# Kernel optimization log

Hardware: AMD Instinct MI355X
Metric: run time of the kernel (lower is better)

Reference implementation:

```python
import jax, jax.numpy as jnp
import numpy as np

B, T, D, H, FA = 512, 64, 128, 128, 64


def setup_inputs() -> dict:
    key = jax.random.key(0)
    ks = jax.random.split(key, 14)
    n = lambda k, s: jax.random.normal(k, s, dtype=jnp.float32) * 0.05
    return {
        "X": jax.random.normal(ks[0], (B, T, D), dtype=jnp.float32),
        "attri_data": jax.random.normal(ks[1], (D, FA), dtype=jnp.float32),
        "w_attr1": n(ks[2], (FA, FA // 2)), "b_attr1": n(ks[3], (FA // 2,)),
        "w_attr2": n(ks[4], (FA // 2, 1)), "b_attr2": n(ks[5], (1,)),
        "w_a1": n(ks[6], (2 * H + T, H)), "b_a1": n(ks[7], (H,)),
        "w_a2": n(ks[8], (H, 1)), "b_a2": n(ks[9], (1,)),
        "w_ih": n(ks[10], (4 * H, D)), "w_hh": n(ks[11], (4 * H, H)),
        "b_ih": n(ks[12], (4 * H,)), "b_hh": n(ks[13], (4 * H,)),
    }


def reference(X, attri_data, w_attr1, b_attr1, w_attr2, b_attr2,
              w_a1, b_a1, w_a2, b_a2, w_ih, w_hh, b_ih, b_hh):
    b, t_dim, d = X.shape
    h_dim = w_hh.shape[1]

    # Attribute attention: softmax over the data_dim axis (dim=0)
    a = attri_data @ w_attr1 + b_attr1
    a = jnp.where(a > 0, a, 0.5 * a)  # LeakyReLU(negative_slope=0.5)
    alpha_attri = jax.nn.softmax(a @ w_attr2 + b_attr2, axis=0)  # [D, 1]
    X_attri = X * alpha_attri.reshape(1, 1, d)  # [B, T, D]
    Xp = jnp.transpose(X_attri, (0, 2, 1))      # [B, D, T] per-variable series

    def step(carry, x_t):  # x_t: [B, D]
        h, c = carry  # [B, H] each; state BEFORE consuming x_t (matches torch loop)
        feat = jnp.concatenate([
            jnp.broadcast_to(h[:, None, :], (b, d, h_dim)),
            jnp.broadcast_to(c[:, None, :], (b, d, h_dim)),
            Xp,
        ], axis=2)  # [B, D, 2H+T]
        e = jnp.tanh(feat @ w_a1 + b_a1) @ w_a2 + b_a2  # [B, D, 1]
        alpha_s = jax.nn.softmax(e[..., 0], axis=1)      # softmax over D
        x_tilde_t = alpha_s * x_t                        # [B, D]
        # LSTM cell (PyTorch gate order i, f, g, o)
        gates = x_t @ w_ih.T + b_ih + h @ w_hh.T + b_hh  # [B, 4H]
        i_g, f_g, g_g, o_g = jnp.split(gates, 4, axis=1)
        c_new = jax.nn.sigmoid(f_g) * c + jax.nn.sigmoid(i_g) * jnp.tanh(g_g)
        h_new = jax.nn.sigmoid(o_g) * jnp.tanh(c_new)
        return (h_new, c_new), x_tilde_t

    h0 = jnp.zeros((b, h_dim), X.dtype)
    c0 = jnp.zeros((b, h_dim), X.dtype)
    _, X_tilde = jax.lax.scan(step, (h0, c0), jnp.transpose(X_attri, (1, 0, 2)))
    return jnp.transpose(X_tilde, (1, 0, 2))  # [B, T, D]
```

## Files before the change

### kernel.cpp

```cpp
#include <hip/hip_runtime.h>
#include <hip/hip_bf16.h>
#include <cstddef>
#include <cstdint>

#define DEVI __device__ __forceinline__

typedef float f32x4 __attribute__((ext_vector_type(4)));
typedef __bf16 bf16x8 __attribute__((ext_vector_type(8)));

DEVI float fast_rcp(float x) { return __builtin_amdgcn_rcpf(x); }
DEVI float sigmoid_fast(float x) { return fast_rcp(1.0f + __expf(-x)); }
DEVI float tanh_fast(float x) { return 1.0f - 2.0f * fast_rcp(__expf(2.0f * x) + 1.0f); }
DEVI float4 ld4(const float* p) { return *reinterpret_cast<const float4*>(p); }
DEVI void st4(float* p, float4 v) { *reinterpret_cast<float4*>(p) = v; }
DEVI float f4c(const float4& v, int i) { return i == 0 ? v.x : i == 1 ? v.y : i == 2 ? v.z : v.w; }
DEVI unsigned short bfbits(float f) { return __builtin_bit_cast(unsigned short, (__bf16)f); }
DEVI unsigned pack2(float a, float b) {
  return (unsigned)bfbits(a) | ((unsigned)bfbits(b) << 16);
}
DEVI f32x4 cvt4(uint2 u) {
  f32x4 r;
  r[0] = __builtin_bit_cast(float, (u.x & 0xffffu) << 16);
  r[1] = __builtin_bit_cast(float, u.x & 0xffff0000u);
  r[2] = __builtin_bit_cast(float, (u.y & 0xffffu) << 16);
  r[3] = __builtin_bit_cast(float, u.y & 0xffff0000u);
  return r;
}
DEVI void barrier_lgkm() {
  __builtin_amdgcn_sched_barrier(0);
  asm volatile("s_waitcnt lgkmcnt(0)" ::: "memory");
  __builtin_amdgcn_s_barrier();
  __builtin_amdgcn_sched_barrier(0);
}

__global__ __launch_bounds__(128) void k_alpha(
    const float* __restrict__ AD, const float* __restrict__ W1,
    const float* __restrict__ B1, const float* __restrict__ W2,
    const float* __restrict__ B2, float* __restrict__ alpha) {
  __shared__ float sW1[64 * 32];
  __shared__ float sW2[32];
  __shared__ float sB1[32];
  __shared__ float red[128];
  __shared__ float s_mx, s_sum;
  int tid = threadIdx.x;
  for (int i = tid; i < 64 * 32; i += 128) sW1[i] = W1[i];
  if (tid < 32) { sW2[tid] = W2[tid]; sB1[tid] = B1[tid]; }
  __syncthreads();
  float ad[64];
  #pragma unroll
  for (int f = 0; f < 64; ++f) ad[f] = AD[tid * 64 + f];
  float logit = B2[0];
  #pragma unroll
  for (int j = 0; j < 32; ++j) {
    float a = sB1[j];
    #pragma unroll
    for (int f = 0; f < 64; ++f) a = fmaf(ad[f], sW1[f * 32 + j], a);
    a = a > 0.0f ? a : 0.5f * a;
    logit = fmaf(a, sW2[j], logit);
  }
  red[tid] = logit;
  __syncthreads();
  if (tid == 0) {
    float mx = red[0];
    for (int i = 1; i < 128; ++i) mx = fmaxf(mx, red[i]);
    float sm = 0.0f;
    for (int i = 0; i < 128; ++i) sm += __expf(red[i] - mx);
    s_mx = mx; s_sum = sm;
  }
  __syncthreads();
  alpha[tid] = __expf(logit - s_mx) / s_sum;
}

__global__ __launch_bounds__(256) void k_wih(
    const float* __restrict__ w_ih, const float* __restrict__ alpha,
    const float* __restrict__ b_ih, const float* __restrict__ b_hh,
    __hip_bfloat16* __restrict__ wA, float* __restrict__ biasJ) {
  int i4 = blockIdx.x * 256 + threadIdx.x;
  int j = i4 >> 5, d0 = (i4 & 31) * 4;
  float4 w = ld4(&w_ih[(size_t)j * 128 + d0]);
  float4 a = ld4(&alpha[d0]);
  uint2 o;
  o.x = pack2(w.x * a.x, w.y * a.y);
  o.y = pack2(w.z * a.z, w.w * a.w);
  *reinterpret_cast<uint2*>(&wA[(size_t)j * 128 + d0]) = o;
  if (i4 < 128) {
    int jb = i4 * 4;
    float4 v0 = ld4(&b_ih[jb]), v1 = ld4(&b_hh[jb]);
    v0.x += v1.x; v0.y += v1.y; v0.z += v1.z; v0.w += v1.w;
    st4(&biasJ[jb], v0);
  }
}

__global__ __launch_bounds__(256) void k_tw(
    const float* __restrict__ w_a1, __hip_bfloat16* __restrict__ w1T) {
  __shared__ float tile[64][132];
  int blk = blockIdx.x;
  int tid = threadIdx.x;
  #pragma unroll
  for (int i = 0; i < 32; ++i) {
    int idx = i * 256 + tid;
    int r = idx >> 7, c = idx & 127;
    tile[r][c] = w_a1[(size_t)(blk * 64 + r) * 128 + c];
  }
  __syncthreads();
  int n = tid >> 1, mh = tid & 1;
  unsigned* dst = reinterpret_cast<unsigned*>(&w1T[(size_t)n * 256 + blk * 64 + mh * 32]);
  #pragma unroll
  for (int i = 0; i < 16; ++i) {
    float a = tile[mh * 32 + 2 * i][n];
    float b = tile[mh * 32 + 2 * i + 1][n];
    dst[i] = pack2(a, b);
  }
}

__global__ __launch_bounds__(256) void k_ep(
    const float* __restrict__ X, const float* __restrict__ w_a1,
    const float* __restrict__ b_a1, const float* __restrict__ alpha,
    float* __restrict__ EP) {
  __shared__ float Xb[64][128];
  __shared__ float Wx[64][128];
  int b = blockIdx.x;
  int tid = threadIdx.x;
  #pragma unroll
  for (int i = 0; i < 8; ++i) {
    int l4 = i * 256 + tid;
    int r = l4 >> 5, c4 = l4 & 31;
    st4(&Xb[r][c4 * 4], ld4(&X[((size_t)b * 64 + r) * 128 + c4 * 4]));
    st4(&Wx[r][c4 * 4], ld4(&w_a1[(size_t)(256 + r) * 128 + c4 * 4]));
  }
  __syncthreads();
  int dg = tid & 15, kg = tid >> 4;
  float acc[8][8] = {};
  #pragma unroll 4
  for (int tau = 0; tau < 64; ++tau) {
    float4 xa0 = ld4(&Xb[tau][dg * 4]);
    float4 xa1 = ld4(&Xb[tau][64 + dg * 4]);
    float4 wa0 = ld4(&Wx[tau][kg * 4]);
    float4 wa1 = ld4(&Wx[tau][64 + kg * 4]);
    #pragma unroll
    for (int i = 0; i < 8; ++i) {
      float xv = (i < 4) ? f4c(xa0, i) : f4c(xa1, i - 4);
      #pragma unroll
      for (int j = 0; j < 4; ++j) {
        acc[i][j]     = fmaf(xv, f4c(wa0, j), acc[i][j]);
        acc[i][j + 4] = fmaf(xv, f4c(wa1, j), acc[i][j + 4]);
      }
    }
  }
  float4 ba0 = ld4(&b_a1[kg * 4]);
  float4 ba1v = ld4(&b_a1[64 + kg * 4]);
  #pragma unroll
  for (int i = 0; i < 8; ++i) {
    int drow = (i < 4) ? dg * 4 + i : 64 + dg * 4 + (i - 4);
    float al = alpha[drow];
    float4 o0, o1;
    float* p0 = &o0.x; float* p1 = &o1.x;
    #pragma unroll
    for (int j = 0; j < 4; ++j) {
      float v0 = 2.0f * fmaf(al, acc[i][j],     f4c(ba0, j));
      float v1 = 2.0f * fmaf(al, acc[i][j + 4], f4c(ba1v, j));
      p0[j] = __expf(fminf(fmaxf(v0, -40.0f), 40.0f));
      p1[j] = __expf(fminf(fmaxf(v1, -40.0f), 40.0f));
    }
    st4(&EP[((size_t)b * 128 + drow) * 128 + kg * 4], o0);
    st4(&EP[((size_t)b * 128 + drow) * 128 + 64 + kg * 4], o1);
  }
}

__global__ __launch_bounds__(256, 2) void k_gxw(
    const float* __restrict__ X, const __hip_bfloat16* __restrict__ wA,
    const float* __restrict__ biasJ, __hip_bfloat16* __restrict__ gx) {
  int rt = blockIdx.x, jt = blockIdx.y;
  int tid = threadIdx.x;
  int wv = tid >> 6, l = tid & 63, lg = l >> 4, lr = l & 15;
  int r0 = rt * 128;
  int j0 = jt * 128 + wv * 32;

  bf16x8 a[2][4];
  #pragma unroll
  for (int ri = 0; ri < 2; ++ri)
    #pragma unroll
    for (int ks = 0; ks < 4; ++ks)
      a[ri][ks] = *reinterpret_cast<const bf16x8*>(
          &wA[(size_t)(j0 + ri * 16 + lr) * 128 + ks * 32 + lg * 8]);

  f32x4 acc[2][8];
  #pragma unroll
  for (int ri = 0; ri < 2; ++ri)
    #pragma unroll
    for (int nj = 0; nj < 8; ++nj) acc[ri][nj] = (f32x4){0.f, 0.f, 0.f, 0.f};

  #pragma unroll 2
  for (int nj = 0; nj < 8; ++nj) {
    bf16x8 bh[4];
    #pragma unroll
    for (int ks = 0; ks < 4; ++ks) {
      const float* src = &X[(size_t)(r0 + nj * 16 + lr) * 128 + ks * 32 + lg * 8];
      float4 f0 = ld4(src), f1 = ld4(src + 4);
      bf16x8 fr;
      fr[0] = (__bf16)f0.x; fr[1] = (__bf16)f0.y;
      fr[2] = (__bf16)f0.z; fr[3] = (__bf16)f0.w;
      fr[4] = (__bf16)f1.x; fr[5] = (__bf16)f1.y;
      fr[6] = (__bf16)f1.z; fr[7] = (__bf16)f1.w;
      bh[ks] = fr;
    }
    #pragma unroll
    for (int ks = 0; ks < 4; ++ks) {
      acc[0][nj] = __builtin_amdgcn_mfma_f32_16x16x32_bf16(a[0][ks], bh[ks], acc[0][nj], 0, 0, 0);
      acc[1][nj] = __builtin_amdgcn_mfma_f32_16x16x32_bf16(a[1][ks], bh[ks], acc[1][nj], 0, 0, 0);
    }
  }

  #pragma unroll
  for (int ri = 0; ri < 2; ++ri) {
    int jb = j0 + ri * 16 + lg * 4;
    float4 bi = ld4(&biasJ[jb]);
    #pragma unroll
    for (int nj = 0; nj < 8; ++nj) {
      int row = r0 + nj * 16 + lr;
      uint2 o;
      o.x = pack2(acc[ri][nj][0] + bi.x, acc[ri][nj][1] + bi.y);
      o.y = pack2(acc[ri][nj][2] + bi.z, acc[ri][nj][3] + bi.w);
      *reinterpret_cast<uint2*>(&gx[(size_t)row * 512 + jb]) = o;
    }
  }
}

__global__ __launch_bounds__(512, 1) void k_rec(
    const __hip_bfloat16* __restrict__ gx, const float* __restrict__ w_hh,
    __hip_bfloat16* __restrict__ S) {
  __shared__ unsigned short kB[2][16 * 128];
  int tid = threadIdx.x;
  int wv = tid >> 6, l = tid & 63, lg = l >> 4, lr = l & 15;
  int b0 = blockIdx.x * 16;

  bf16x8 ah[4][4];
  #pragma unroll
  for (int ks = 0; ks < 4; ++ks)
    #pragma unroll
    for (int q = 0; q < 4; ++q) {
      const float* src = &w_hh[(size_t)(q * 128 + wv * 16 + lr) * 128 + ks * 32 + lg * 8];
      float4 f0 = ld4(src), f1 = ld4(src + 4);
      bf16x8 fr;
      fr[0] = (__bf16)f0.x; fr[1] = (__bf16)f0.y;
      fr[2] = (__bf16)f0.z; fr[3] = (__bf16)f0.w;
      fr[4] = (__bf16)f1.x; fr[5] = (__bf16)f1.y;
      fr[6] = (__bf16)f1.z; fr[7] = (__bf16)f1.w;
      ah[ks][q] = fr;
    }

  alignas(16) float hA[4] = {0.f, 0.f, 0.f, 0.f};
  alignas(16) float cA[4] = {0.f, 0.f, 0.f, 0.f};
  int m0 = wv * 16 + lg * 4;
  int wIdx = lr * 128 + (((m0 >> 3) ^ lr) << 3) + (m0 & 7);
  const __hip_bfloat16* gxb = gx + (size_t)(b0 + lr) * 64 * 512 + wv * 16 + lg * 4;

  uint2 z; z.x = 0u; z.y = 0u;
  *reinterpret_cast<uint2*>(&kB[0][wIdx]) = z;
  uint2 gA[4], gB[4];
  #pragma unroll
  for (int q = 0; q < 4; ++q) gA[q] = *reinterpret_cast<const uint2*>(gxb + q * 128);
  #pragma unroll
  for (int q = 0; q < 4; ++q) gB[q] = *reinterpret_cast<const uint2*>(gxb + 512 + q * 128);
  __syncthreads();

#define REC_STEP(T, SRC, DST, G)                                               \
  do {                                                                         \
    int t_ = (T);                                                              \
    bf16x8 bh[4];                                                              \
    _Pragma("unroll")                                                          \
    for (int ks = 0; ks < 4; ++ks)                                             \
      bh[ks] = *reinterpret_cast<const bf16x8*>(                               \
          &kB[SRC][lr * 128 + ((((ks << 2) + lg) ^ lr) << 3)]);                \
    f32x4 ac0 = cvt4(G[0]), ac1 = cvt4(G[1]), ac2 = cvt4(G[2]), ac3 = cvt4(G[3]); \
    int tn_ = t_ + 2 < 64 ? t_ + 2 : 63;                                       \
    _Pragma("unroll")                                                          \
    for (int q = 0; q < 4; ++q)                                                \
      G[q] = *reinterpret_cast<const uint2*>(gxb + (size_t)tn_ * 512 + q * 128); \
    {                                                                          \
      uint2 hS; hS.x = pack2(hA[0], hA[1]); hS.y = pack2(hA[2], hA[3]);        \
      uint2 cS; cS.x = pack2(cA[0], cA[1]); cS.y = pack2(cA[2], cA[3]);        \
      __hip_bfloat16* sp = S + ((size_t)(t_ * 512) + b0 + lr) * 256 + m0;      \
      *reinterpret_cast<uint2*>(sp) = hS;                                      \
      *reinterpret_cast<uint2*>(sp + 128) = cS;                                \
    }                                                                          \
    _Pragma("unroll")                                                          \
    for (int ks = 0; ks < 4; ++ks) {                                           \
      ac0 = __builtin_amdgcn_mfma_f32_16x16x32_bf16(ah[ks][0], bh[ks], ac0, 0, 0, 0); \
      ac1 = __builtin_amdgcn_mfma_f32_16x16x32_bf16(ah[ks][1], bh[ks], ac1, 0, 0, 0); \
      ac2 = __builtin_amdgcn_mfma_f32_16x16x32_bf16(ah[ks][2], bh[ks], ac2, 0, 0, 0); \
      ac3 = __builtin_amdgcn_mfma_f32_16x16x32_bf16(ah[ks][3], bh[ks], ac3, 0, 0, 0); \
    }                                                                          \
    _Pragma("unroll")                                                          \
    for (int r = 0; r < 4; ++r) {                                              \
      float ig = sigmoid_fast(ac0[r]);                                         \
      float fg = sigmoid_fast(ac1[r]);                                         \
      float gg = tanh_fast(ac2[r]);                                            \
      float og = sigmoid_fast(ac3[r]);                                         \
      float cn = fmaf(fg, cA[r], ig * gg);                                     \
      float hn = og * tanh_fast(cn);                                           \
      cA[r] = cn; hA[r] = hn;                                                  \
    }                                                                          \
    {                                                                          \
      uint2 hu; hu.x = pack2(hA[0], hA[1]); hu.y = pack2(hA[2], hA[3]);        \
      *reinterpret_cast<uint2*>(&kB[DST][wIdx]) = hu;                          \
    }                                                                          \
    barrier_lgkm();                                                            \
  } while (0)

  #pragma unroll 1
  for (int it = 0; it < 32; ++it) {
    REC_STEP(2 * it, 0, 1, gA);
    REC_STEP(2 * it + 1, 1, 0, gB);
  }
#undef REC_STEP
}

__global__ __launch_bounds__(256, 1) void k_eq(
    const __hip_bfloat16* __restrict__ S, const __hip_bfloat16* __restrict__ w1T,
    float* __restrict__ EQ) {
  int tid = threadIdx.x;
  int wv = tid >> 6, l = tid & 63;
  int lr = l & 15, lg = l >> 4;
  int r0 = blockIdx.x * 128 + wv * 32;

  bf16x8 a[2][8];
  #pragma unroll
  for (int ri = 0; ri < 2; ++ri)
    #pragma unroll
    for (int ks = 0; ks < 8; ++ks)
      a[ri][ks] = *reinterpret_cast<const bf16x8*>(
          &S[(size_t)(r0 + ri * 16 + lr) * 256 + ks * 32 + lg * 8]);

  f32x4 acc[2][8];
  #pragma unroll
  for (int ri = 0; ri < 2; ++ri)
    #pragma unroll
    for (int nj = 0; nj < 8; ++nj) acc[ri][nj] = (f32x4){0.f, 0.f, 0.f, 0.f};

  #pragma unroll
  for (int nj = 0; nj < 8; ++nj) {
    bf16x8 bf[8];
    #pragma unroll
    for (int ks = 0; ks < 8; ++ks)
      bf[ks] = *reinterpret_cast<const bf16x8*>(
          &w1T[(size_t)(nj * 16 + lr) * 256 + ks * 32 + lg * 8]);
    #pragma unroll
    for (int ks = 0; ks < 8; ++ks) {
      acc[0][nj] = __builtin_amdgcn_mfma_f32_16x16x32_bf16(a[0][ks], bf[ks], acc[0][nj], 0, 0, 0);
      acc[1][nj] = __builtin_amdgcn_mfma_f32_16x16x32_bf16(a[1][ks], bf[ks], acc[1][nj], 0, 0, 0);
    }
  }

  #pragma unroll
  for (int ri = 0; ri < 2; ++ri)
    #pragma unroll
    for (int nj = 0; nj < 8; ++nj)
      #pragma unroll
      for (int r = 0; r < 4; ++r) {
        int grow = r0 + ri * 16 + lg * 4 + r;
        int n = nj * 16 + lr;
        float v = 2.0f * acc[ri][nj][r];
        EQ[(size_t)grow * 128 + n] = __expf(fminf(fmaxf(v, -40.f), 40.f));
      }
}

__global__ __launch_bounds__(512, 2) void k_attn(
    const float* __restrict__ EP, const float* __restrict__ EQ,
    const float* __restrict__ w_a2, const float* __restrict__ alpha,
    const float* __restrict__ X, float* __restrict__ out) {
  __shared__ float EQs[64][128];
  __shared__ float e_lds[8][128];
  int b = blockIdx.x;
  int tid = threadIdx.x;
  #pragma unroll
  for (int i = 0; i < 4; ++i) {
    int l4 = i * 512 + tid;
    int t = l4 >> 5, k4 = l4 & 31;
    st4(&EQs[t][k4 * 4], ld4(&EQ[((size_t)t * 512 + b) * 128 + k4 * 4]));
  }
  int d = tid >> 2, s = tid & 3;
  float4 ep[8], w2r[8];
  #pragma unroll
  for (int q = 0; q < 8; ++q) {
    ep[q]  = ld4(&EP[((size_t)b * 128 + d) * 128 + s * 32 + q * 4]);
    w2r[q] = ld4(&w_a2[s * 32 + q * 4]);
  }
  int wv = tid >> 6, l = tid & 63;
  float al0 = alpha[l], al1 = alpha[64 + l];
  barrier_lgkm();

  for (int rnd = 0; rnd < 8; ++rnd) {
    #pragma unroll
    for (int it = 0; it < 8; ++it) {
      int t = rnd * 8 + it;
      float p = 0.0f;
      #pragma unroll
      for (int q = 0; q < 8; ++q) {
        float4 eq = ld4(&EQs[t][s * 32 + q * 4]);
        p = fmaf(w2r[q].x, fast_rcp(fmaf(ep[q].x, eq.x, 1.0f)), p);
        p = fmaf(w2r[q].y, fast_rcp(fmaf(ep[q].y, eq.y, 1.0f)), p);
        p = fmaf(w2r[q].z, fast_rcp(fmaf(ep[q].z, eq.z, 1.0f)), p);
        p = fmaf(w2r[q].w, fast_rcp(fmaf(ep[q].w, eq.w, 1.0f)), p);
      }
      p += __shfl_xor(p, 1);
      p += __shfl_xor(p, 2);
      if (s == 0) e_lds[it][d] = -2.0f * p;
    }
    barrier_lgkm();
    {
      int t = rnd * 8 + wv;
      float v0 = e_lds[wv][l], v1 = e_lds[wv][64 + l];
      float mx = fmaxf(v0, v1);
      #pragma unroll
      for (int o = 1; o < 64; o <<= 1) mx = fmaxf(mx, __shfl_xor(mx, o));
      float e0 = __expf(v0 - mx), e1 = __expf(v1 - mx);
      float sm = e0 + e1;
      #pragma unroll
      for (int o = 1; o < 64; o <<= 1) sm += __shfl_xor(sm, o);
      float inv = fast_rcp(sm);
      size_t ro = ((size_t)b * 64 + t) * 128;
      out[ro + l]      = e0 * inv * al0 * X[ro + l];
      out[ro + 64 + l] = e1 * inv * al1 * X[ro + 64 + l];
    }
    barrier_lgkm();
  }
}

extern "C" void kernel_launch(void* const* d_in, const int* in_sizes, int n_in,
                              void* d_out, int out_size, void* d_ws, size_t ws_size,
                              hipStream_t stream) {
  const float* X    = (const float*)d_in[0];
  const float* AD   = (const float*)d_in[1];
  const float* W1   = (const float*)d_in[2];
  const float* B1   = (const float*)d_in[3];
  const float* W2   = (const float*)d_in[4];
  const float* B2   = (const float*)d_in[5];
  const float* w_a1 = (const float*)d_in[6];
  const float* b_a1 = (const float*)d_in[7];
  const float* w_a2 = (const float*)d_in[8];
  const float* w_ih = (const float*)d_in[10];
  const float* w_hh = (const float*)d_in[11];
  const float* b_ih = (const float*)d_in[12];
  const float* b_hh = (const float*)d_in[13];
  float* out = (float*)d_out;
  float* ws = (float*)d_ws;

  float* alpha = ws;
  float* EQ    = ws + 256;
  float* EP    = EQ + 4194304;
  float* fS    = EP + 8388608;
  __hip_bfloat16* S = (__hip_bfloat16*)fS;
  float* fgx   = fS + 4194304;
  __hip_bfloat16* gx = (__hip_bfloat16*)fgx;
  float* fw1T  = fgx + 8388608;
  __hip_bfloat16* w1T = (__hip_bfloat16*)fw1T;
  float* fwA   = fw1T + 16384;
  __hip_bfloat16* wA = (__hip_bfloat16*)fwA;
  float* biasJ = fwA + 32768;

  hipLaunchKernelGGL(k_alpha, dim3(1),   dim3(128), 0, stream, AD, W1, B1, W2, B2, alpha);
  hipLaunchKernelGGL(k_wih,   dim3(64),  dim3(256), 0, stream, w_ih, alpha, b_ih, b_hh, wA, biasJ);
  hipLaunchKernelGGL(k_tw,    dim3(4),   dim3(256), 0, stream, w_a1, w1T);
  hipLaunchKernelGGL(k_ep,    dim3(512), dim3(256), 0, stream, X, w_a1, b_a1, alpha, EP);
  hipLaunchKernelGGL(k_gxw,   dim3(256, 4), dim3(256), 0, stream, X, wA, biasJ, gx);
  hipLaunchKernelGGL(k_rec,   dim3(32),  dim3(512), 0, stream, gx, w_hh, S);
  hipLaunchKernelGGL(k_eq,    dim3(256), dim3(256), 0, stream, S, w1T, EQ);
  hipLaunchKernelGGL(k_attn,  dim3(512), dim3(512), 0, stream, EP, EQ, w_a2, alpha, X, out);
}
```

Before: 362.9 us.

## Fuse prep kernels, fold EQ projection into recurrence, co-schedule EP blocks

Merges the alpha, w_ih scaling and w_a1 transpose kernels into one prep launch, with each block recomputing alpha redundantly. The hidden/cell state projection that produced EQ now runs inside the recurrent kernel through extra MFMAs on the LDS-resident h and c, which removes the S buffer round trip and the separate k_eq launch. The EP computation runs as extra blocks of the same launch so it can overlap the 32 latency-bound recurrence blocks. The cost is more work and LDS traffic per recurrence step on the serial critical path, plus redundant alpha computation in 64 blocks.

```diff
diff --git a/kernel.cpp b/kernel.cpp
--- a/kernel.cpp
+++ b/kernel.cpp
@@ -33,137 +33,87 @@
   __builtin_amdgcn_sched_barrier(0);
 }
 
-__global__ __launch_bounds__(128) void k_alpha(
+__global__ __launch_bounds__(256) void k_prep(
     const float* __restrict__ AD, const float* __restrict__ W1,
     const float* __restrict__ B1, const float* __restrict__ W2,
-    const float* __restrict__ B2, float* __restrict__ alpha) {
-  __shared__ float sW1[64 * 32];
-  __shared__ float sW2[32];
-  __shared__ float sB1[32];
-  __shared__ float red[128];
-  __shared__ float s_mx, s_sum;
-  int tid = threadIdx.x;
-  for (int i = tid; i < 64 * 32; i += 128) sW1[i] = W1[i];
-  if (tid < 32) { sW2[tid] = W2[tid]; sB1[tid] = B1[tid]; }
-  __syncthreads();
-  float ad[64];
-  #pragma unroll
-  for (int f = 0; f < 64; ++f) ad[f] = AD[tid * 64 + f];
-  float logit = B2[0];
-  #pragma unroll
-  for (int j = 0; j < 32; ++j) {
-    float a = sB1[j];
-    #pragma unroll
-    for (int f = 0; f < 64; ++f) a = fmaf(ad[f], sW1[f * 32 + j], a);
-    a = a > 0.0f ? a : 0.5f * a;
-    logit = fmaf(a, sW2[j], logit);
-  }
-  red[tid] = logit;
-  __syncthreads();
-  if (tid == 0) {
-    float mx = red[0];
-    for (int i = 1; i < 128; ++i) mx = fmaxf(mx, red[i]);
-    float sm = 0.0f;
-    for (int i = 0; i < 128; ++i) sm += __expf(red[i] - mx);
-    s_mx = mx; s_sum = sm;
-  }
-  __syncthreads();
-  alpha[tid] = __expf(logit - s_mx) / s_sum;
-}
-
-__global__ __launch_bounds__(256) void k_wih(
-    const float* __restrict__ w_ih, const float* __restrict__ alpha,
+    const float* __restrict__ B2, const float* __restrict__ w_ih,
     const float* __restrict__ b_ih, const float* __restrict__ b_hh,
-    __hip_bfloat16* __restrict__ wA, float* __restrict__ biasJ) {
-  int i4 = blockIdx.x * 256 + threadIdx.x;
-  int j = i4 >> 5, d0 = (i4 & 31) * 4;
-  float4 w = ld4(&w_ih[(size_t)j * 128 + d0]);
-  float4 a = ld4(&alpha[d0]);
-  uint2 o;
-  o.x = pack2(w.x * a.x, w.y * a.y);
-  o.y = pack2(w.z * a.z, w.w * a.w);
-  *reinterpret_cast<uint2*>(&wA[(size_t)j * 128 + d0]) = o;
-  if (i4 < 128) {
-    int jb = i4 * 4;
-    float4 v0 = ld4(&b_ih[jb]), v1 = ld4(&b_hh[jb]);
-    v0.x += v1.x; v0.y += v1.y; v0.z += v1.z; v0.w += v1.w;
-    st4(&biasJ[jb], v0);
-  }
-}
-
-__global__ __launch_bounds__(256) void k_tw(
-    const float* __restrict__ w_a1, __hip_bfloat16* __restrict__ w1T) {
-  __shared__ float tile[64][132];
-  int blk = blockIdx.x;
-  int tid = threadIdx.x;
-  #pragma unroll
-  for (int i = 0; i < 32; ++i) {
-    int idx = i * 256 + tid;
-    int r = idx >> 7, c = idx & 127;
-    tile[r][c] = w_a1[(size_t)(blk * 64 + r) * 128 + c];
-  }
-  __syncthreads();
-  int n = tid >> 1, mh = tid & 1;
-  unsigned* dst = reinterpret_cast<unsigned*>(&w1T[(size_t)n * 256 + blk * 64 + mh * 32]);
-  #pragma unroll
-  for (int i = 0; i < 16; ++i) {
-    float a = tile[mh * 32 + 2 * i][n];
-    float b = tile[mh * 32 + 2 * i + 1][n];
-    dst[i] = pack2(a, b);
-  }
-}
-
-__global__ __launch_bounds__(256) void k_ep(
-    const float* __restrict__ X, const float* __restrict__ w_a1,
-    const float* __restrict__ b_a1, const float* __restrict__ alpha,
-    float* __restrict__ EP) {
-  __shared__ float Xb[64][128];
-  __shared__ float Wx[64][128];
-  int b = blockIdx.x;
-  int tid = threadIdx.x;
-  #pragma unroll
-  for (int i = 0; i < 8; ++i) {
-    int l4 = i * 256 + tid;
-    int r = l4 >> 5, c4 = l4 & 31;
-    st4(&Xb[r][c4 * 4], ld4(&X[((size_t)b * 64 + r) * 128 + c4 * 4]));
-    st4(&Wx[r][c4 * 4], ld4(&w_a1[(size_t)(256 + r) * 128 + c4 * 4]));
-  }
-  __syncthreads();
-  int dg = tid & 15, kg = tid >> 4;
-  float acc[8][8] = {};
-  #pragma unroll 4
-  for (int tau = 0; tau < 64; ++tau) {
-    float4 xa0 = ld4(&Xb[tau][dg * 4]);
-    float4 xa1 = ld4(&Xb[tau][64 + dg * 4]);
-    float4 wa0 = ld4(&Wx[tau][kg * 4]);
-    float4 wa1 = ld4(&Wx[tau][64 + kg * 4]);
-    #pragma unroll
-    for (int i = 0; i < 8; ++i) {
-      float xv = (i < 4) ? f4c(xa0, i) : f4c(xa1, i - 4);
-      #pragma unroll
-      for (int j = 0; j < 4; ++j) {
-        acc[i][j]     = fmaf(xv, f4c(wa0, j), acc[i][j]);
-        acc[i][j + 4] = fmaf(xv, f4c(wa1, j), acc[i][j + 4]);
+    const float* __restrict__ w_a1, float* __restrict__ alpha_g,
+    __hip_bfloat16* __restrict__ wA, float* __restrict__ biasJ,
+    __hip_bfloat16* __restrict__ w1T) {
+  __shared__ float sh[64 * 132];
+  int bid = blockIdx.x, tid = threadIdx.x;
+  if (bid < 64) {
+    float* sW1 = sh;
+    float* sW2 = sh + 2048;
+    float* sB1 = sh + 2080;
+    float* red = sh + 2112;
+    float* sA  = sh + 2240;
+    float* sMS = sh + 2368;
+    for (int i = tid; i < 2048; i += 256) sW1[i] = W1[i];
+    if (tid < 32) { sW2[tid] = W2[tid]; sB1[tid] = B1[tid]; }
+    __syncthreads();
+    if (tid < 128) {
+      float ad[64];
+      #pragma unroll
+      for (int f = 0; f < 64; ++f) ad[f] = AD[tid * 64 + f];
+      float logit = B2[0];
+      #pragma unroll
+      for (int j = 0; j < 32; ++j) {
+        float a = sB1[j];
+        #pragma unroll
+        for (int f = 0; f < 64; ++f) a = fmaf(ad[f], sW1[f * 32 + j], a);
+        a = a > 0.0f ? a : 0.5f * a;
+        logit = fmaf(a, sW2[j], logit);
       }
-    }
-  }
-  float4 ba0 = ld4(&b_a1[kg * 4]);
-  float4 ba1v = ld4(&b_a1[64 + kg * 4]);
-  #pragma unroll
-  for (int i = 0; i < 8; ++i) {
-    int drow = (i < 4) ? dg * 4 + i : 64 + dg * 4 + (i - 4);
-    float al = alpha[drow];
-    float4 o0, o1;
-    float* p0 = &o0.x; float* p1 = &o1.x;
-    #pragma unroll
-    for (int j = 0; j < 4; ++j) {
-      float v0 = 2.0f * fmaf(al, acc[i][j],     f4c(ba0, j));
-      float v1 = 2.0f * fmaf(al, acc[i][j + 4], f4c(ba1v, j));
-      p0[j] = __expf(fminf(fmaxf(v0, -40.0f), 40.0f));
-      p1[j] = __expf(fminf(fmaxf(v1, -40.0f), 40.0f));
-    }
-    st4(&EP[((size_t)b * 128 + drow) * 128 + kg * 4], o0);
-    st4(&EP[((size_t)b * 128 + drow) * 128 + 64 + kg * 4], o1);
+      red[tid] = logit;
+    }
+    __syncthreads();
+    if (tid == 0) {
+      float mx = red[0];
+      for (int i = 1; i < 128; ++i) mx = fmaxf(mx, red[i]);
+      float sm = 0.0f;
+      for (int i = 0; i < 128; ++i) sm += __expf(red[i] - mx);
+      sMS[0] = mx; sMS[1] = sm;
+    }
+    __syncthreads();
+    if (tid < 128) {
+      float a = __expf(red[tid] - sMS[0]) / sMS[1];
+      sA[tid] = a;
+      if (bid == 0) alpha_g[tid] = a;
+    }
+    __syncthreads();
+    int i4 = bid * 256 + tid;
+    int j = i4 >> 5, d0 = (i4 & 31) * 4;
+    float4 w = ld4(&w_ih[(size_t)j * 128 + d0]);
+    uint2 o;
+    o.x = pack2(w.x * sA[d0], w.y * sA[d0 + 1]);
+    o.y = pack2(w.z * sA[d0 + 2], w.w * sA[d0 + 3]);
+    *reinterpret_cast<uint2*>(&wA[(size_t)j * 128 + d0]) = o;
+    if (i4 < 128) {
+      int jb = i4 * 4;
+      float4 v0 = ld4(&b_ih[jb]), v1 = ld4(&b_hh[jb]);
+      v0.x += v1.x; v0.y += v1.y; v0.z += v1.z; v0.w += v1.w;
+      st4(&biasJ[jb], v0);
+    }
+  } else {
+    float (*tile)[132] = reinterpret_cast<float(*)[132]>(sh);
+    int blk = bid - 64;
+    #pragma unroll
+    for (int i = 0; i < 32; ++i) {
+      int idx = i * 256 + tid;
+      int r = idx >> 7, c = idx & 127;
+      tile[r][c] = w_a1[(size_t)(blk * 64 + r) * 128 + c];
+    }
+    __syncthreads();
+    int n = tid >> 1, mh = tid & 1;
+    unsigned* dst = reinterpret_cast<unsigned*>(&w1T[(size_t)n * 256 + blk * 64 + mh * 32]);
+    #pragma unroll
+    for (int i = 0; i < 16; ++i) {
+      float a = tile[mh * 32 + 2 * i][n];
+      float b = tile[mh * 32 + 2 * i + 1][n];
+      dst[i] = pack2(a, b);
+    }
   }
 }
 
@@ -226,13 +176,64 @@
   }
 }
 
-__global__ __launch_bounds__(512, 1) void k_rec(
+__global__ __launch_bounds__(512, 1) void k_recep(
     const __hip_bfloat16* __restrict__ gx, const float* __restrict__ w_hh,
-    __hip_bfloat16* __restrict__ S) {
-  __shared__ unsigned short kB[2][16 * 128];
+    const __hip_bfloat16* __restrict__ w1T, float* __restrict__ EQ,
+    const float* __restrict__ X, const float* __restrict__ w_a1,
+    const float* __restrict__ b_a1, const float* __restrict__ alpha_g,
+    float* __restrict__ EP) {
+  __shared__ float shmem[2 * 64 * 128];
+  int bid = blockIdx.x;
   int tid = threadIdx.x;
+
+  if (bid >= 32) {
+    int b = bid - 32;
+    float (*Xb)[128] = reinterpret_cast<float(*)[128]>(&shmem[0]);
+    float (*Wx)[128] = reinterpret_cast<float(*)[128]>(&shmem[8192]);
+    #pragma unroll
+    for (int i = 0; i < 4; ++i) {
+      int l4 = i * 512 + tid;
+      int r = l4 >> 5, c4 = l4 & 31;
+      st4(&Xb[r][c4 * 4], ld4(&X[((size_t)b * 64 + r) * 128 + c4 * 4]));
+      st4(&Wx[r][c4 * 4], ld4(&w_a1[(size_t)(256 + r) * 128 + c4 * 4]));
+    }
+    __syncthreads();
+    int dg = tid & 15, kg = tid >> 4;
+    float acc[8][4] = {};
+    #pragma unroll 4
+    for (int tau = 0; tau < 64; ++tau) {
+      float4 xa0 = ld4(&Xb[tau][dg * 4]);
+      float4 xa1 = ld4(&Xb[tau][64 + dg * 4]);
+      float4 wa = ld4(&Wx[tau][kg * 4]);
+      #pragma unroll
+      for (int i = 0; i < 8; ++i) {
+        float xv = (i < 4) ? f4c(xa0, i) : f4c(xa1, i - 4);
+        #pragma unroll
+        for (int j = 0; j < 4; ++j)
+          acc[i][j] = fmaf(xv, f4c(wa, j), acc[i][j]);
+      }
+    }
+    float4 ba = ld4(&b_a1[kg * 4]);
+    #pragma unroll
+    for (int i = 0; i < 8; ++i) {
+      int drow = (i < 4) ? dg * 4 + i : 64 + dg * 4 + (i - 4);
+      float al = alpha_g[drow];
+      float4 o;
+      float* po = &o.x;
+      #pragma unroll
+      for (int j = 0; j < 4; ++j) {
+        float v = 2.0f * fmaf(al, acc[i][j], f4c(ba, j));
+        po[j] = __expf(fminf(fmaxf(v, -40.0f), 40.0f));
+      }
+      st4(&EP[((size_t)b * 128 + drow) * 128 + kg * 4], o);
+    }
+    return;
+  }
+
+  unsigned short* kBp = reinterpret_cast<unsigned short*>(shmem);
+  unsigned short* kCp = kBp + 4096;
   int wv = tid >> 6, l = tid & 63, lg = l >> 4, lr = l & 15;
-  int b0 = blockIdx.x * 16;
+  int b0 = bid * 16;
 
   bf16x8 ah[4][4];
   #pragma unroll
@@ -249,6 +250,12 @@
       ah[ks][q] = fr;
     }
 
+  bf16x8 wt[8];
+  #pragma unroll
+  for (int ks = 0; ks < 8; ++ks)
+    wt[ks] = *reinterpret_cast<const bf16x8*>(
+        &w1T[(size_t)(wv * 16 + lr) * 256 + ks * 32 + lg * 8]);
+
   alignas(16) float hA[4] = {0.f, 0.f, 0.f, 0.f};
   alignas(16) float cA[4] = {0.f, 0.f, 0.f, 0.f};
   int m0 = wv * 16 + lg * 4;
@@ -256,7 +263,8 @@
   const __hip_bfloat16* gxb = gx + (size_t)(b0 + lr) * 64 * 512 + wv * 16 + lg * 4;
 
   uint2 z; z.x = 0u; z.y = 0u;
-  *reinterpret_cast<uint2*>(&kB[0][wIdx]) = z;
+  *reinterpret_cast<uint2*>(&kBp[wIdx]) = z;
+  *reinterpret_cast<uint2*>(&kCp[wIdx]) = z;
   uint2 gA[4], gB[4];
   #pragma unroll
   for (int q = 0; q < 4; ++q) gA[q] = *reinterpret_cast<const uint2*>(gxb + q * 128);
@@ -267,29 +275,41 @@
 #define REC_STEP(T, SRC, DST, G)                                               \
   do {                                                                         \
     int t_ = (T);                                                              \
-    bf16x8 bh[4];                                                              \
-    _Pragma("unroll")                                                          \
-    for (int ks = 0; ks < 4; ++ks)                                             \
-      bh[ks] = *reinterpret_cast<const bf16x8*>(                               \
-          &kB[SRC][lr * 128 + ((((ks << 2) + lg) ^ lr) << 3)]);                \
+    bf16x8 bh[4], bc[4];                                                       \
+    _Pragma("unroll")                                                          \
+    for (int ks = 0; ks < 4; ++ks) {                                           \
+      int idx_ = lr * 128 + ((((ks << 2) + lg) ^ lr) << 3);                    \
+      bh[ks] = *reinterpret_cast<const bf16x8*>(&kBp[(SRC) * 2048 + idx_]);    \
+      bc[ks] = *reinterpret_cast<const bf16x8*>(&kCp[(SRC) * 2048 + idx_]);    \
+    }                                                                          \
     f32x4 ac0 = cvt4(G[0]), ac1 = cvt4(G[1]), ac2 = cvt4(G[2]), ac3 = cvt4(G[3]); \
     int tn_ = t_ + 2 < 64 ? t_ + 2 : 63;                                       \
     _Pragma("unroll")                                                          \
     for (int q = 0; q < 4; ++q)                                                \
       G[q] = *reinterpret_cast<const uint2*>(gxb + (size_t)tn_ * 512 + q * 128); \
-    {                                                                          \
-      uint2 hS; hS.x = pack2(hA[0], hA[1]); hS.y = pack2(hA[2], hA[3]);        \
-      uint2 cS; cS.x = pack2(cA[0], cA[1]); cS.y = pack2(cA[2], cA[3]);        \
-      __hip_bfloat16* sp = S + ((size_t)(t_ * 512) + b0 + lr) * 256 + m0;      \
-      *reinterpret_cast<uint2*>(sp) = hS;                                      \
-      *reinterpret_cast<uint2*>(sp + 128) = cS;                                \
-    }                                                                          \
+    f32x4 ea = (f32x4){0.f, 0.f, 0.f, 0.f};                                    \
     _Pragma("unroll")                                                          \
     for (int ks = 0; ks < 4; ++ks) {                                           \
       ac0 = __builtin_amdgcn_mfma_f32_16x16x32_bf16(ah[ks][0], bh[ks], ac0, 0, 0, 0); \
       ac1 = __builtin_amdgcn_mfma_f32_16x16x32_bf16(ah[ks][1], bh[ks], ac1, 0, 0, 0); \
       ac2 = __builtin_amdgcn_mfma_f32_16x16x32_bf16(ah[ks][2], bh[ks], ac2, 0, 0, 0); \
       ac3 = __builtin_amdgcn_mfma_f32_16x16x32_bf16(ah[ks][3], bh[ks], ac3, 0, 0, 0); \
+    }                                                                          \
+    _Pragma("unroll")                                                          \
+    for (int ks = 0; ks < 4; ++ks)                                             \
+      ea = __builtin_amdgcn_mfma_f32_16x16x32_bf16(wt[ks], bh[ks], ea, 0, 0, 0); \
+    _Pragma("unroll")                                                          \
+    for (int ks = 0; ks < 4; ++ks)                                             \
+      ea = __builtin_amdgcn_mfma_f32_16x16x32_bf16(wt[ks + 4], bc[ks], ea, 0, 0, 0); \
+    {                                                                          \
+      float4 eo;                                                               \
+      float* pe = &eo.x;                                                       \
+      _Pragma("unroll")                                                        \
+      for (int r = 0; r < 4; ++r) {                                            \
+        float v = 2.0f * ea[r];                                                \
+        pe[r] = __expf(fminf(fmaxf(v, -40.0f), 40.0f));                        \
+      }                                                                        \
+      st4(&EQ[((size_t)(t_ * 512) + b0 + lr) * 128 + wv * 16 + lg * 4], eo);   \
     }                                                                          \
     _Pragma("unroll")                                                          \
     for (int r = 0; r < 4; ++r) {                                              \
@@ -303,7 +323,9 @@
     }                                                                          \
     {                                                                          \
       uint2 hu; hu.x = pack2(hA[0], hA[1]); hu.y = pack2(hA[2], hA[3]);        \
-      *reinterpret_cast<uint2*>(&kB[DST][wIdx]) = hu;                          \
+      uint2 cu; cu.x = pack2(cA[0], cA[1]); cu.y = pack2(cA[2], cA[3]);        \
+      *reinterpret_cast<uint2*>(&kBp[(DST) * 2048 + wIdx]) = hu;               \
+      *reinterpret_cast<uint2*>(&kCp[(DST) * 2048 + wIdx]) = cu;               \
     }                                                                          \
     barrier_lgkm();                                                            \
   } while (0)
@@ -314,55 +336,6 @@
     REC_STEP(2 * it + 1, 1, 0, gB);
   }
 #undef REC_STEP
-}
-
-__global__ __launch_bounds__(256, 1) void k_eq(
-    const __hip_bfloat16* __restrict__ S, const __hip_bfloat16* __restrict__ w1T,
-    float* __restrict__ EQ) {
-  int tid = threadIdx.x;
-  int wv = tid >> 6, l = tid & 63;
-  int lr = l & 15, lg = l >> 4;
-  int r0 = blockIdx.x * 128 + wv * 32;
-
-  bf16x8 a[2][8];
-  #pragma unroll
-  for (int ri = 0; ri < 2; ++ri)
-    #pragma unroll
-    for (int ks = 0; ks < 8; ++ks)
-      a[ri][ks] = *reinterpret_cast<const bf16x8*>(
-          &S[(size_t)(r0 + ri * 16 + lr) * 256 + ks * 32 + lg * 8]);
-
-  f32x4 acc[2][8];
-  #pragma unroll
-  for (int ri = 0; ri < 2; ++ri)
-    #pragma unroll
-    for (int nj = 0; nj < 8; ++nj) acc[ri][nj] = (f32x4){0.f, 0.f, 0.f, 0.f};
-
-  #pragma unroll
-  for (int nj = 0; nj < 8; ++nj) {
-    bf16x8 bf[8];
-    #pragma unroll
-    for (int ks = 0; ks < 8; ++ks)
-      bf[ks] = *reinterpret_cast<const bf16x8*>(
-          &w1T[(size_t)(nj * 16 + lr) * 256 + ks * 32 + lg * 8]);
-    #pragma unroll
-    for (int ks = 0; ks < 8; ++ks) {
-      acc[0][nj] = __builtin_amdgcn_mfma_f32_16x16x32_bf16(a[0][ks], bf[ks], acc[0][nj], 0, 0, 0);
-      acc[1][nj] = __builtin_amdgcn_mfma_f32_16x16x32_bf16(a[1][ks], bf[ks], acc[1][nj], 0, 0, 0);
-    }
-  }
-
-  #pragma unroll
-  for (int ri = 0; ri < 2; ++ri)
-    #pragma unroll
-    for (int nj = 0; nj < 8; ++nj)
-      #pragma unroll
-      for (int r = 0; r < 4; ++r) {
-        int grow = r0 + ri * 16 + lg * 4 + r;
-        int n = nj * 16 + lr;
-        float v = 2.0f * acc[ri][nj][r];
-        EQ[(size_t)grow * 128 + n] = __expf(fminf(fmaxf(v, -40.f), 40.f));
-      }
 }
 
 __global__ __launch_bounds__(512, 2) void k_attn(
@@ -388,7 +361,7 @@
   }
   int wv = tid >> 6, l = tid & 63;
   float al0 = alpha[l], al1 = alpha[64 + l];
-  barrier_lgkm();
+  __syncthreads();
 
   for (int rnd = 0; rnd < 8; ++rnd) {
     #pragma unroll
@@ -407,7 +380,7 @@
       p += __shfl_xor(p, 2);
       if (s == 0) e_lds[it][d] = -2.0f * p;
     }
-    barrier_lgkm();
+    __syncthreads();
     {
       int t = rnd * 8 + wv;
       float v0 = e_lds[wv][l], v1 = e_lds[wv][64 + l];
@@ -423,7 +396,7 @@
       out[ro + l]      = e0 * inv * al0 * X[ro + l];
       out[ro + 64 + l] = e1 * inv * al1 * X[ro + 64 + l];
     }
-    barrier_lgkm();
+    __syncthreads();
   }
 }
 
@@ -449,9 +422,7 @@
   float* alpha = ws;
   float* EQ    = ws + 256;
   float* EP    = EQ + 4194304;
-  float* fS    = EP + 8388608;
-  __hip_bfloat16* S = (__hip_bfloat16*)fS;
-  float* fgx   = fS + 4194304;
+  float* fgx   = EP + 8388608;
   __hip_bfloat16* gx = (__hip_bfloat16*)fgx;
   float* fw1T  = fgx + 8388608;
   __hip_bfloat16* w1T = (__hip_bfloat16*)fw1T;
@@ -459,12 +430,12 @@
   __hip_bfloat16* wA = (__hip_bfloat16*)fwA;
   float* biasJ = fwA + 32768;
 
-  hipLaunchKernelGGL(k_alpha, dim3(1),   dim3(128), 0, stream, AD, W1, B1, W2, B2, alpha);
-  hipLaunchKernelGGL(k_wih,   dim3(64),  dim3(256), 0, stream, w_ih, alpha, b_ih, b_hh, wA, biasJ);
-  hipLaunchKernelGGL(k_tw,    dim3(4),   dim3(256), 0, stream, w_a1, w1T);
-  hipLaunchKernelGGL(k_ep,    dim3(512), dim3(256), 0, stream, X, w_a1, b_a1, alpha, EP);
-  hipLaunchKernelGGL(k_gxw,   dim3(256, 4), dim3(256), 0, stream, X, wA, biasJ, gx);
-  hipLaunchKernelGGL(k_rec,   dim3(32),  dim3(512), 0, stream, gx, w_hh, S);
-  hipLaunchKernelGGL(k_eq,    dim3(256), dim3(256), 0, stream, S, w1T, EQ);
-  hipLaunchKernelGGL(k_attn,  dim3(512), dim3(512), 0, stream, EP, EQ, w_a2, alpha, X, out);
-}
+  hipLaunchKernelGGL(k_prep,  dim3(68),      dim3(256), 0, stream,
+                     AD, W1, B1, W2, B2, w_ih, b_ih, b_hh, w_a1,
+                     alpha, wA, biasJ, w1T);
+  hipLaunchKernelGGL(k_gxw,   dim3(256, 4),  dim3(256), 0, stream, X, wA, biasJ, gx);
+  hipLaunchKernelGGL(k_recep, dim3(544),     dim3(512), 0, stream,
+                     gx, w_hh, w1T, EQ, X, w_a1, b_a1, alpha, EP);
+  hipLaunchKernelGGL(k_attn,  dim3(512),     dim3(512), 0, stream,
+                     EP, EQ, w_a2, alpha, X, out);
+}
```

Result: faster. 331.0 us (-8.8%).
